# Performance work log

Hardware: AMD Instinct MI355X
Metric: run time of the kernel (lower is better)

Reference implementation:

```python
import jax, jax.numpy as jnp
import numpy as np

HEADS = 8
NEG_SLOPE = 0.2


def _layer_norm(x, g, b, eps=1e-5):
    mu = x.mean(-1, keepdims=True)
    var = ((x - mu) ** 2).mean(-1, keepdims=True)
    return (x - mu) / jnp.sqrt(var + eps) * g + b


def setup_inputs() -> dict:
    key = jax.random.key(0)
    ks = jax.random.split(key, 24)
    N, E, H, L = 512, 260000, 256, 4
    s = 0.05
    return dict(
        x=jax.random.normal(ks[0], (N, 1), jnp.float32),
        edge_index=jax.random.randint(ks[1], (2, E), 0, N),
        edge_attr=jax.random.uniform(ks[2], (E, 3), jnp.float32),
        emb_W=jax.random.normal(ks[3], (1, H)) * s,
        emb_b=jnp.zeros((H,)),
        Wl=jax.random.normal(ks[4], (L, H, H)) * s,
        bl=jnp.zeros((L, H)),
        Wr=jax.random.normal(ks[5], (L, H, H)) * s,
        br=jnp.zeros((L, H)),
        We=jax.random.normal(ks[6], (L, 3, H)) * s,
        att=jax.random.normal(ks[7], (L, HEADS, H // HEADS)) * s,
        gb=jnp.zeros((L, H)),
        ln_g=jnp.ones((L, H)),
        ln_b=jnp.zeros((L, H)),
        p1_W=jax.random.normal(ks[8], (2 * H, H)) * s,
        p1_b=jnp.zeros((H,)),
        p2_W=jax.random.normal(ks[9], (H, H // 2)) * s,
        p2_b=jnp.zeros((H // 2,)),
        p3_W=jax.random.normal(ks[10], (H // 2, 1)) * s,
        p3_b=jnp.zeros((1,)),
        v1_W=jax.random.normal(ks[11], (2 * H, H)) * s,
        v1_b=jnp.zeros((H,)),
        v2_W=jax.random.normal(ks[12], (H, 1)) * s,
        v2_b=jnp.zeros((1,)),
        coupling=jnp.asarray(1.0, jnp.float32),
    )


def reference(x, edge_index, edge_attr, emb_W, emb_b, Wl, bl, Wr, br, We, att,
              gb, ln_g, ln_b, p1_W, p1_b, p2_W, p2_b, p3_W, p3_b,
              v1_W, v1_b, v2_W, v2_b, coupling):
    N = x.shape[0]
    E = edge_attr.shape[0]
    L = Wl.shape[0]
    C = Wl.shape[-1] // HEADS
    src, dst = edge_index[0], edge_index[1]

    # PyG GATv2Conv adds self-loops with edge_attr fill_value='mean'
    # (mean of incoming edge_attr per destination node).
    sums = jax.ops.segment_sum(edge_attr, dst, num_segments=N)
    cnt = jax.ops.segment_sum(jnp.ones((E,), edge_attr.dtype), dst, num_segments=N)
    self_attr = sums / jnp.maximum(cnt, 1.0)[:, None]
    loop = jnp.arange(N)
    src_f = jnp.concatenate([src, loop])            # [E+N]
    dst_f = jnp.concatenate([dst, loop])
    ea_f = jnp.concatenate([edge_attr, self_attr])  # [E+N, 3]

    h = x @ emb_W + emb_b                           # [N, H]
    for l in range(L):
        res = h
        xl = (h @ Wl[l] + bl[l]).reshape(N, HEADS, C)
        xr = (h @ Wr[l] + br[l]).reshape(N, HEADS, C)
        ee = (ea_f @ We[l]).reshape(-1, HEADS, C)
        # GATv2 scoring: leaky_relu(x_l[src]+x_r[dst]+edge) . att
        m = jax.nn.leaky_relu(xl[src_f] + xr[dst_f] + ee, NEG_SLOPE)
        alpha = jnp.einsum('ehc,hc->eh', m, att[l])
        amax = jax.ops.segment_max(alpha, dst_f, num_segments=N)
        alpha = jnp.exp(alpha - amax[dst_f])
        denom = jax.ops.segment_sum(alpha, dst_f, num_segments=N)
        alpha = alpha / denom[dst_f]
        out = jax.ops.segment_sum(xl[src_f] * alpha[..., None], dst_f,
                                  num_segments=N).reshape(N, HEADS * C) + gb[l]
        h = jax.nn.relu(_layer_norm(out + res, ln_g[l], ln_b[l]))

    # graph-level representation (single graph, batch=None branch)
    graph_repr = jnp.concatenate([h.mean(0, keepdims=True),
                                  h.max(0, keepdims=True)], axis=1)  # [1, 2H]

    # all-pairs edge representations (i < j)
    iu, ju = jnp.triu_indices(N, k=1)
    er = jnp.concatenate([h[iu], h[ju]], axis=1)    # [N(N-1)/2, 2H]
    p = jax.nn.relu(er @ p1_W + p1_b)
    p = jax.nn.relu(p @ p2_W + p2_b)
    policy_logits = (p @ p3_W + p3_b).squeeze(-1)   # [N(N-1)/2]

    v = jax.nn.relu(graph_repr @ v1_W + v1_b)
    value = (v @ v2_W + v2_b).squeeze(-1)           # [1]

    # Potts energy: per-color degree-squared approximation of triangles
    colors = jnp.argmax(edge_attr, axis=1)
    energy = jnp.asarray(0.0, h.dtype)
    for c in (1, 2):
        w = (colors == c).astype(h.dtype)
        deg = (jax.ops.segment_sum(w, src, num_segments=N)
               + jax.ops.segment_sum(w, dst, num_segments=N))
        energy = energy + (deg ** 2).sum() / (2.0 * N)
    energy = energy * coupling

    return policy_logits, value, energy
```

## Files before the change

### kernel.cpp

```cpp
#include <hip/hip_runtime.h>
#include <math.h>

#define HDIM 256
#define NHEADS 8
#define NEG 0.2f
#define NB 64
#define SEG 4

typedef float f32x4 __attribute__((ext_vector_type(4)));
typedef _Float16 f16x8 __attribute__((ext_vector_type(8)));
typedef __fp16 fp16v2 __attribute__((ext_vector_type(2)));

__global__ __launch_bounds__(256) void edge_part(
    const int* __restrict__ ei, const float* __restrict__ ea, int E, int CH,
    int* __restrict__ pcnt, float* __restrict__ psum, int* __restrict__ pcol) {
  __shared__ int   lcnt[512];
  __shared__ float ls0[512], ls1[512], ls2[512];
  __shared__ int   lcol[1024];
  int t = threadIdx.x, b = blockIdx.x;
  for (int n = t; n < 512; n += 256) {
    lcnt[n] = 0; ls0[n] = 0.f; ls1[n] = 0.f; ls2[n] = 0.f;
    lcol[n] = 0; lcol[512 + n] = 0;
  }
  __syncthreads();
  int e0 = b * CH, e1 = min(E, e0 + CH);
  for (int e = e0 + t; e < e1; e += 256) {
    int src = ei[e], dst = ei[E + e];
    float a0 = ea[3*e], a1 = ea[3*e+1], a2 = ea[3*e+2];
    atomicAdd(&lcnt[dst], 1);
    atomicAdd(&ls0[dst], a0);
    atomicAdd(&ls1[dst], a1);
    atomicAdd(&ls2[dst], a2);
    int idx = 0; float best = a0;
    if (a1 > best) { best = a1; idx = 1; }
    if (a2 > best) { idx = 2; }
    if (idx) {
      int o = (idx - 1) << 9;
      atomicAdd(&lcol[o + src], 1);
      atomicAdd(&lcol[o + dst], 1);
    }
  }
  __syncthreads();
  for (int n = t; n < 512; n += 256) {
    pcnt[b*512 + n] = lcnt[n];
    psum[(size_t)(0*NB + b)*512 + n] = ls0[n];
    psum[(size_t)(1*NB + b)*512 + n] = ls1[n];
    psum[(size_t)(2*NB + b)*512 + n] = ls2[n];
    pcol[(size_t)(0*NB + b)*512 + n] = lcol[n];
    pcol[(size_t)(1*NB + b)*512 + n] = lcol[512 + n];
  }
}

__global__ __launch_bounds__(256) void red_kernel(
    const int* __restrict__ pcnt, const float* __restrict__ psum,
    const int* __restrict__ pcol,
    int* __restrict__ cnt, float* __restrict__ sred, int* __restrict__ dred,
    int* __restrict__ pbase) {
  int q = blockIdx.x >> 1;
  int n = (blockIdx.x & 1)*256 + threadIdx.x;
  if (q == 0) {
    int run = 0;
#pragma unroll 8
    for (int b = 0; b < NB; ++b) {
      int v = pcnt[b*512 + n];
      pbase[b*512 + n] = run;
      run += v;
    }
    cnt[n] = run;
  } else if (q <= 3) {
    int qq = q - 1;
    float s = 0.f;
#pragma unroll 8
    for (int b = 0; b < NB; ++b) s += psum[(size_t)(qq*NB + b)*512 + n];
    sred[qq*512 + n] = s;
  } else {
    int qq = q - 4;
    int s = 0;
#pragma unroll 8
    for (int b = 0; b < NB; ++b) s += pcol[(size_t)(qq*NB + b)*512 + n];
    dred[qq*512 + n] = s;
  }
}

__global__ __launch_bounds__(512) void scan2(
    const int* __restrict__ cnt, const float* __restrict__ sred,
    const int* __restrict__ dred, int N,
    int* __restrict__ rowp, float4* __restrict__ csr,
    const float* __restrict__ coupling, float* __restrict__ eout) {
  int t = threadIdx.x;
  int c = (t < N) ? cnt[t] : 0;
  __shared__ int sbuf[512];
  int v = (t < N) ? (c + 1) : 0;
  sbuf[t] = v;
  __syncthreads();
  for (int off = 1; off < 512; off <<= 1) {
    int add = (t >= off) ? sbuf[t - off] : 0;
    __syncthreads();
    sbuf[t] += add;
    __syncthreads();
  }
  int incl = sbuf[t], excl = incl - v;
  if (t < N) {
    rowp[t] = excl;
    if (t == N - 1) rowp[N] = incl;
    float inv = 1.f / fmaxf((float)c, 1.f);
    csr[excl] = make_float4(sred[t]*inv, sred[512 + t]*inv, sred[1024 + t]*inv,
                            __int_as_float(t));
  }
  float e = 0.f;
  if (t < N) {
    float d1 = (float)dred[t], d2 = (float)dred[512 + t];
    e = d1*d1 + d2*d2;
  }
#pragma unroll
  for (int off = 1; off < 64; off <<= 1) e += __shfl_xor(e, off);
  __shared__ float wred[8];
  if ((t & 63) == 0) wred[t >> 6] = e;
  __syncthreads();
  if (t == 0) {
    float s = 0.f;
#pragma unroll
    for (int i = 0; i < 8; ++i) s += wred[i];
    eout[0] = coupling[0] * s / (2.f * (float)N);
  }
}

__global__ __launch_bounds__(256) void scatter2(
    const int* __restrict__ ei, const float* __restrict__ ea, int E, int CH,
    const int* __restrict__ rowp, const int* __restrict__ pbase,
    float4* __restrict__ csr) {
  __shared__ int lofs[512];
  int t = threadIdx.x, b = blockIdx.x;
  for (int n = t; n < 512; n += 256) lofs[n] = 0;
  __syncthreads();
  int e0 = b * CH, e1 = min(E, e0 + CH);
  for (int e = e0 + t; e < e1; e += 256) {
    int src = ei[e], dst = ei[E + e];
    float a0 = ea[3*e], a1 = ea[3*e+1], a2 = ea[3*e+2];
    int lp = atomicAdd(&lofs[dst], 1);
    int pos = rowp[dst] + 1 + pbase[b*512 + dst] + lp;
    csr[pos] = make_float4(a0, a1, a2, __int_as_float(src));
  }
}

__global__ __launch_bounds__(256) void emb_kernel(
    const float* __restrict__ x, const float* __restrict__ eW,
    const float* __restrict__ eb, float* __restrict__ h) {
  int n = blockIdx.x, t = threadIdx.x;
  h[n*HDIM + t] = fmaf(x[n], eW[t], eb[t]);
}

__global__ __launch_bounds__(256) void dual_gemm(
    const float* __restrict__ Hm,
    const float* __restrict__ W1, const float* __restrict__ b1,
    const float* __restrict__ W2, const float* __restrict__ b2,
    float* __restrict__ o1, float* __restrict__ o2) {
  int t = threadIdx.x;
  int n0 = blockIdx.x * 2;
  __shared__ float sh[2][HDIM];
#pragma unroll
  for (int r = 0; r < 2; ++r) sh[r][t] = Hm[(size_t)(n0 + r)*HDIM + t];
  __syncthreads();
  float a[2] = {0.f,0.f}, b[2] = {0.f,0.f};
#pragma unroll 8
  for (int k = 0; k < HDIM; ++k) {
    float w1 = W1[(size_t)k*HDIM + t];
    float w2 = W2[(size_t)k*HDIM + t];
#pragma unroll
    for (int r = 0; r < 2; ++r) {
      a[r] = fmaf(sh[r][k], w1, a[r]);
      b[r] = fmaf(sh[r][k], w2, b[r]);
    }
  }
  float bb1 = b1 ? b1[t] : 0.f;
  float bb2 = b2 ? b2[t] : 0.f;
#pragma unroll
  for (int r = 0; r < 2; ++r) {
    o1[(size_t)(n0 + r)*HDIM + t] = a[r] + bb1;
    o2[(size_t)(n0 + r)*HDIM + t] = b[r] + bb2;
  }
}

__global__ __launch_bounds__(256) void attn_gather(
    const float* __restrict__ xl, const float* __restrict__ xr,
    const float4* __restrict__ csr, const int* __restrict__ row_start,
    const float* __restrict__ We, const float* __restrict__ att,
    float* __restrict__ pm, float* __restrict__ pl, float* __restrict__ pacc) {
  int nb = blockIdx.x;
  int n = nb >> 2, sgm = nb & (SEG - 1);
  int t = threadIdx.x;
  int g = t >> 5, l = t & 31, hd = l >> 2, qd = l & 3;
  int cb = hd*32 + qd*8;

  float xrv[8], w0[8], w1[8], w2[8], av[8];
#pragma unroll
  for (int j = 0; j < 8; ++j) {
    xrv[j] = xr[(size_t)n*HDIM + cb + j];
    w0[j]  = We[cb + j];
    w1[j]  = We[HDIM + cb + j];
    w2[j]  = We[2*HDIM + cb + j];
    av[j]  = att[cb + j];
  }
  int rs = row_start[n], re = row_start[n+1], len = re - rs;
  int s0 = rs + ((len * sgm) >> 2);
  int s1 = rs + ((len * (sgm + 1)) >> 2);

  float mh = -INFINITY, lh = 0.f;
  float acc[8] = {0.f,0.f,0.f,0.f,0.f,0.f,0.f,0.f};

  int idx = s0 + g;
  if (idx < s1) {
    float4 rec = csr[idx];
    while (idx < s1) {
      int idxn = idx + 8;
      float4 recn = csr[idxn < s1 ? idxn : rs];
      int s = __float_as_int(rec.w);
      const float* xp = xl + (size_t)s*HDIM + cb;
      float xv[8];
      float4 x0 = *(const float4*)xp;
      float4 x1 = *(const float4*)(xp + 4);
      xv[0]=x0.x; xv[1]=x0.y; xv[2]=x0.z; xv[3]=x0.w;
      xv[4]=x1.x; xv[5]=x1.y; xv[6]=x1.z; xv[7]=x1.w;
      float partial = 0.f;
#pragma unroll
      for (int j = 0; j < 8; ++j) {
        float m = fmaf(rec.z, w2[j], fmaf(rec.y, w1[j], fmaf(rec.x, w0[j], xrv[j]))) + xv[j];
        m = fmaxf(m, NEG * m);
        partial = fmaf(m, av[j], partial);
      }
      partial += __shfl_xor(partial, 1);
      partial += __shfl_xor(partial, 2);
      if (partial > mh) {
        float sc = __expf(mh - partial);
        lh *= sc;
#pragma unroll
        for (int j = 0; j < 8; ++j) acc[j] *= sc;
        mh = partial;
      }
      float pw = __expf(partial - mh);
      lh += pw;
#pragma unroll
      for (int j = 0; j < 8; ++j) acc[j] = fmaf(pw, xv[j], acc[j]);
      rec = recn; idx = idxn;
    }
  }

  __shared__ float lacc[8][HDIM];
  __shared__ float lm[8][NHEADS];
  __shared__ float llv[8][NHEADS];
#pragma unroll
  for (int j = 0; j < 8; ++j) lacc[g][cb + j] = acc[j];
  if (qd == 0) { lm[g][hd] = mh; llv[g][hd] = lh; }
  __syncthreads();

  int c = t, hh = c >> 5;
  float M = -INFINITY;
#pragma unroll
  for (int g2 = 0; g2 < 8; ++g2) M = fmaxf(M, lm[g2][hh]);
  float L = 0.f, o = 0.f;
#pragma unroll
  for (int g2 = 0; g2 < 8; ++g2) {
    float e2 = __expf(lm[g2][hh] - M);
    L = fmaf(llv[g2][hh], e2, L);
    o = fmaf(lacc[g2][c], e2, o);
  }
  pacc[(size_t)nb*HDIM + c] = o;
  if ((c & 31) == 0) {
    pm[nb*NHEADS + hh] = M;
    pl[nb*NHEADS + hh] = L;
  }
}

__global__ __launch_bounds__(256) void attn_merge(
    const float* __restrict__ pm, const float* __restrict__ pl,
    const float* __restrict__ pacc,
    const float* __restrict__ gb, const float* __restrict__ lng,
    const float* __restrict__ lnb,
    const float* __restrict__ h_in, float* __restrict__ h_out) {
  int n = blockIdx.x, t = threadIdx.x;
  int c = t, hh = c >> 5;
  float M = -INFINITY;
#pragma unroll
  for (int s = 0; s < SEG; ++s) M = fmaxf(M, pm[(n*SEG + s)*NHEADS + hh]);
  float L = 0.f, o = 0.f;
#pragma unroll
  for (int s = 0; s < SEG; ++s) {
    float e2 = __expf(pm[(n*SEG + s)*NHEADS + hh] - M);
    L = fmaf(pl[(n*SEG + s)*NHEADS + hh], e2, L);
    o = fmaf(pacc[(size_t)(n*SEG + s)*HDIM + c], e2, o);
  }
  float val = o / L + gb[c] + h_in[(size_t)n*HDIM + c];

  float s1 = val, s2 = val * val;
#pragma unroll
  for (int off = 1; off < 64; off <<= 1) {
    s1 += __shfl_xor(s1, off);
    s2 += __shfl_xor(s2, off);
  }
  __shared__ float rs1[4], rs2[4];
  if ((t & 63) == 0) { rs1[t >> 6] = s1; rs2[t >> 6] = s2; }
  __syncthreads();
  float S1 = rs1[0] + rs1[1] + rs1[2] + rs1[3];
  float S2 = rs2[0] + rs2[1] + rs2[2] + rs2[3];
  float mu = S1 * (1.f/HDIM);
  float var = S2 * (1.f/HDIM) - mu * mu;
  float y = (val - mu) * rsqrtf(var + 1e-5f);
  y = fmaf(y, lng[c], lnb[c]);
  h_out[(size_t)n*HDIM + c] = fmaxf(y, 0.f);
}

__global__ __launch_bounds__(256) void w2_prep_kernel(
    const float* __restrict__ W2, unsigned short* __restrict__ W2h) {
  int tid = blockIdx.x * 256 + threadIdx.x;
  int k = tid >> 7, n = tid & 127;
  int c = k >> 5, kq = (k >> 3) & 3, kj = k & 7;
  int nt = n >> 4, nl = n & 15;
  int lane = kq*16 + nl;
  _Float16 hv = (_Float16)W2[(size_t)k*128 + n];
  W2h[(size_t)(((c*8 + nt)*64 + lane)*8 + kj)] = *(unsigned short*)&hv;
}

__global__ __launch_bounds__(256, 4) void pair_mfma_kernel(
    const float* __restrict__ A, const float* __restrict__ Bm,
    const unsigned short* __restrict__ W2h,
    const float* __restrict__ b2, const float* __restrict__ W3,
    const float* __restrict__ b3, float* __restrict__ out, int N) {
  int bb = blockIdx.x;
  int half = bb & 1;
  int b = bb >> 1, ti = 0, rem = 32;
  while (b >= rem) { b -= rem; ti++; rem--; }
  int tj = ti + b;
  int i0 = ti * 16 + half * 8;
  int j0 = tj * 16;

  int t = threadIdx.x;
  int w = t >> 6, l = t & 63;
  int quad = l >> 4, nl = l & 15;

  float b2v[8], w3v[8];
#pragma unroll
  for (int nt = 0; nt < 8; ++nt) {
    b2v[nt] = b2[nt*16 + nl];
    w3v[nt] = W3[nt*16 + nl];
  }

  const float* Brow = Bm + (size_t)(j0 + nl) * HDIM;
  const float* Arow0 = A + (size_t)(i0 + w*2) * HDIM;

  f32x4 acc[2][8];
#pragma unroll
  for (int a2 = 0; a2 < 2; ++a2)
#pragma unroll
    for (int nt = 0; nt < 8; ++nt) acc[a2][nt] = (f32x4){0.f,0.f,0.f,0.f};

  for (int c = 0; c < 8; ++c) {
    int kb = c*32 + quad*8;
    float4 bv0 = *(const float4*)(Brow + kb);
    float4 bv1 = *(const float4*)(Brow + kb + 4);

    f16x8 afrag[2];
#pragma unroll
    for (int a2 = 0; a2 < 2; ++a2) {
      const float* Ar = Arow0 + (size_t)a2*HDIM + kb;
      float4 av0 = *(const float4*)Ar;
      float4 av1 = *(const float4*)(Ar + 4);
      union { f16x8 v8; fp16v2 v2[4]; } u;
      u.v2[0] = __builtin_amdgcn_cvt_pkrtz(fmaxf(av0.x + bv0.x, 0.f),
                                           fmaxf(av0.y + bv0.y, 0.f));
      u.v2[1] = __builtin_amdgcn_cvt_pkrtz(fmaxf(av0.z + bv0.z, 0.f),
                                           fmaxf(av0.w + bv0.w, 0.f));
      u.v2[2] = __builtin_amdgcn_cvt_pkrtz(fmaxf(av1.x + bv1.x, 0.f),
                                           fmaxf(av1.y + bv1.y, 0.f));
      u.v2[3] = __builtin_amdgcn_cvt_pkrtz(fmaxf(av1.z + bv1.z, 0.f),
                                           fmaxf(av1.w + bv1.w, 0.f));
      afrag[a2] = u.v8;
    }

#pragma unroll
    for (int nt = 0; nt < 8; ++nt) {
      f16x8 bfrag = *(const f16x8*)(W2h + (size_t)(((c*8 + nt)*64 + l) * 8));
#pragma unroll
      for (int a2 = 0; a2 < 2; ++a2)
        acc[a2][nt] = __builtin_amdgcn_mfma_f32_16x16x32_f16(
            afrag[a2], bfrag, acc[a2][nt], 0, 0, 0);
    }
  }

  float b3v = b3[0];
#pragma unroll
  for (int a2 = 0; a2 < 2; ++a2) {
    int i = i0 + w*2 + a2;
#pragma unroll
    for (int r = 0; r < 4; ++r) {
      float s = 0.f;
#pragma unroll
      for (int nt = 0; nt < 8; ++nt)
        s = fmaf(fmaxf(acc[a2][nt][r] + b2v[nt], 0.f), w3v[nt], s);
      s += __shfl_xor(s, 1);
      s += __shfl_xor(s, 2);
      s += __shfl_xor(s, 4);
      s += __shfl_xor(s, 8);
      if (nl == 0) {
        int j = j0 + quad*4 + r;
        if (i < j)
          out[(size_t)i*(2*N - i - 1)/2 + (j - i - 1)] = s + b3v;
      }
    }
  }
}

__global__ __launch_bounds__(256) void pool_kernel(
    const float* __restrict__ h, float* __restrict__ psums,
    float* __restrict__ pmaxs) {
  int g = blockIdx.x, t = threadIdx.x;
  float s = 0.f, m = -INFINITY;
#pragma unroll
  for (int r = 0; r < 16; ++r) {
    float v = h[(size_t)(g*16 + r)*HDIM + t];
    s += v; m = fmaxf(m, v);
  }
  psums[g*HDIM + t] = s;
  pmaxs[g*HDIM + t] = m;
}

__global__ __launch_bounds__(256) void value1_kernel(
    const float* __restrict__ psums, const float* __restrict__ pmaxs,
    const float* __restrict__ v1W, float* __restrict__ vpart, int N) {
  int b = blockIdx.x, t = threadIdx.x;
  int k0 = b * 16;
  int kk = t >> 4, g = t & 15;
  __shared__ float repr16[16];
  int k = k0 + kk;
  float v;
  if (k < HDIM) {
    v = psums[g*HDIM + k] + psums[(g + 16)*HDIM + k];
    v += __shfl_xor(v, 1); v += __shfl_xor(v, 2);
    v += __shfl_xor(v, 4); v += __shfl_xor(v, 8);
    if (g == 0) repr16[kk] = v / (float)N;
  } else {
    int kc = k - HDIM;
    v = fmaxf(pmaxs[g*HDIM + kc], pmaxs[(g + 16)*HDIM + kc]);
    v = fmaxf(v, __shfl_xor(v, 1)); v = fmaxf(v, __shfl_xor(v, 2));
    v = fmaxf(v, __shfl_xor(v, 4)); v = fmaxf(v, __shfl_xor(v, 8));
    if (g == 0) repr16[kk] = v;
  }
  __syncthreads();
  float pv = 0.f;
#pragma unroll
  for (int q = 0; q < 16; ++q)
    pv = fmaf(repr16[q], v1W[(size_t)(k0 + q)*HDIM + t], pv);
  vpart[b*HDIM + t] = pv;
}

__global__ __launch_bounds__(256) void value2_kernel(
    const float* __restrict__ vpart, const float* __restrict__ v1b,
    const float* __restrict__ v2W, const float* __restrict__ v2b,
    float* __restrict__ out) {
  int t = threadIdx.x;
  float a = 0.f;
#pragma unroll
  for (int g = 0; g < 32; ++g) a += vpart[g*HDIM + t];
  a = fmaxf(a + v1b[t], 0.f);
  float pv = a * v2W[t];
#pragma unroll
  for (int off = 1; off < 64; off <<= 1) pv += __shfl_xor(pv, off);
  __shared__ float wsum[4];
  if ((t & 63) == 0) wsum[t >> 6] = pv;
  __syncthreads();
  if (t == 0) out[0] = wsum[0] + wsum[1] + wsum[2] + wsum[3] + v2b[0];
}

extern "C" void kernel_launch(void* const* d_in, const int* in_sizes, int n_in,
                              void* d_out, int out_size, void* d_ws, size_t ws_size,
                              hipStream_t stream) {
  const float* x    = (const float*)d_in[0];
  const int*   ei   = (const int*)  d_in[1];
  const float* ea   = (const float*)d_in[2];
  const float* embW = (const float*)d_in[3];
  const float* embb = (const float*)d_in[4];
  const float* Wl   = (const float*)d_in[5];
  const float* bl   = (const float*)d_in[6];
  const float* Wr   = (const float*)d_in[7];
  const float* br   = (const float*)d_in[8];
  const float* We   = (const float*)d_in[9];
  const float* att  = (const float*)d_in[10];
  const float* gb   = (const float*)d_in[11];
  const float* lng  = (const float*)d_in[12];
  const float* lnb  = (const float*)d_in[13];
  const float* p1W  = (const float*)d_in[14];
  const float* p1b  = (const float*)d_in[15];
  const float* p2W  = (const float*)d_in[16];
  const float* p2b  = (const float*)d_in[17];
  const float* p3W  = (const float*)d_in[18];
  const float* p3b  = (const float*)d_in[19];
  const float* v1W  = (const float*)d_in[20];
  const float* v1b  = (const float*)d_in[21];
  const float* v2W  = (const float*)d_in[22];
  const float* v2b  = (const float*)d_in[23];
  const float* coup = (const float*)d_in[24];

  int N = in_sizes[0];
  int E = in_sizes[2] / 3;
  float* out = (float*)d_out;
  size_t P = (size_t)N*(N-1)/2;

  char* w = (char*)d_ws;
  int*    rowp = (int*)   (w + 0);
  float*  plS  = (float*) (w + 2560);
  float*  plM  = (float*) (w + 35328);
  float*  vprt = (float*) (w + 68096);
  float4* csr  = (float4*)(w + 101120);
  size_t csr_end = 101120 + (size_t)(E + N) * 16;
  csr_end = (csr_end + 255) & ~(size_t)255;
  float* hA  = (float*)(w + csr_end);
  float* hB  = hA  + (size_t)N*HDIM;
  float* xlb = hB  + (size_t)N*HDIM;
  float* xrb = xlb + (size_t)N*HDIM;
  float* Ab  = xrb + (size_t)N*HDIM;
  float* Bb  = Ab  + (size_t)N*HDIM;
  unsigned short* W2h = (unsigned short*)(Bb + (size_t)N*HDIM);
  size_t ubase = ((size_t)((char*)(W2h + 32768) - w) + 255) & ~(size_t)255;

  char* U = w + ubase;
  int*    pcnt = (int*)   (U + 0);
  float*  psum = (float*) (U + 131072);
  int*    pcol = (int*)   (U + 524288);
  int*    pbase= (int*)   (U + 786432);
  int*    cnt  = (int*)   (U + 917504);
  float*  sred = (float*) (U + 919552);
  int*    dred = (int*)   (U + 925696);
  float*  pmv  = (float*) (U + 0);
  float*  plv  = (float*) (U + 65536);
  float*  pacc = (float*) (U + 131072);

  int CH = (E + NB - 1) / NB;
  edge_part<<<NB, 256, 0, stream>>>(ei, ea, E, CH, pcnt, psum, pcol);
  red_kernel<<<12, 256, 0, stream>>>(pcnt, psum, pcol, cnt, sred, dred, pbase);
  scan2<<<1, 512, 0, stream>>>(cnt, sred, dred, N, rowp, csr, coup, out + P + 1);
  scatter2<<<NB, 256, 0, stream>>>(ei, ea, E, CH, rowp, pbase, csr);
  emb_kernel<<<N, 256, 0, stream>>>(x, embW, embb, hA);
  w2_prep_kernel<<<128, 256, 0, stream>>>(p2W, W2h);

  float* hin = hA;
  float* hout = hB;
  for (int l = 0; l < 4; ++l) {
    dual_gemm<<<N/2, 256, 0, stream>>>(hin,
        Wl + (size_t)l*HDIM*HDIM, bl + l*HDIM,
        Wr + (size_t)l*HDIM*HDIM, br + l*HDIM, xlb, xrb);
    attn_gather<<<N*SEG, 256, 0, stream>>>(xlb, xrb, csr, rowp,
        We + (size_t)l*3*HDIM, att + (size_t)l*HDIM, pmv, plv, pacc);
    attn_merge<<<N, 256, 0, stream>>>(pmv, plv, pacc,
        gb + (size_t)l*HDIM, lng + (size_t)l*HDIM, lnb + (size_t)l*HDIM,
        hin, hout);
    float* tmp = hin; hin = hout; hout = tmp;
  }

  dual_gemm<<<N/2, 256, 0, stream>>>(hin, p1W, p1b,
      p1W + (size_t)HDIM*HDIM, (const float*)nullptr, Ab, Bb);

  pair_mfma_kernel<<<1056, 256, 0, stream>>>(Ab, Bb, W2h, p2b, p3W, p3b, out, N);

  pool_kernel<<<32, 256, 0, stream>>>(hin, plS, plM);
  value1_kernel<<<32, 256, 0, stream>>>(plS, plM, v1W, vprt, N);
  value2_kernel<<<1, 256, 0, stream>>>(vprt, v1b, v2W, v2b, out + P);
}
```

Baseline: 351.3 us.

## Use fp16 MFMA for per-layer dual GEMMs with pre-swizzled weights

Replaces the scalar fp32 dual_gemm with an MFMA 16x16x32 fp16 kernel. A new prep kernel converts all Wl, Wr and p1 weights once into fp16 in the MFMA B-fragment layout. Activations are converted to fp16 on the fly with round-toward-zero packing. This targets the five small 512x256x256 GEMM pairs, at the cost of an extra prep launch and reduced precision in the node projections.

Result: faster. 319.5 us (-9.0%).

```diff
diff --git a/kernel.cpp b/kernel.cpp
--- a/kernel.cpp
+++ b/kernel.cpp
@@ -150,35 +150,57 @@
   h[n*HDIM + t] = fmaf(x[n], eW[t], eb[t]);
 }
 
-__global__ __launch_bounds__(256) void dual_gemm(
+__global__ __launch_bounds__(256) void w_prep_all(
+    const float* __restrict__ Wl, const float* __restrict__ Wr,
+    const float* __restrict__ p1W, unsigned short* __restrict__ dst) {
+  int gid = blockIdx.x * 256 + threadIdx.x;
+  int s = gid >> 16, e = gid & 65535;
+  int k = e >> 8, n = e & 255;
+  const float* src = (s < 4) ? (Wl + (size_t)s*65536)
+                   : (s < 8) ? (Wr + (size_t)(s-4)*65536)
+                             : (p1W + (size_t)(s-8)*65536);
+  int c = k >> 5, quad = (k >> 3) & 3, kj = k & 7;
+  int nt = n >> 4, nl = n & 15;
+  int lane = quad*16 + nl;
+  _Float16 hv = (_Float16)src[(size_t)k*256 + n];
+  dst[(size_t)s*65536 + ((nt*8 + c)*512 + lane*8 + kj)] = *(unsigned short*)&hv;
+}
+
+__global__ __launch_bounds__(256) void dual_gemm_mfma(
     const float* __restrict__ Hm,
-    const float* __restrict__ W1, const float* __restrict__ b1,
-    const float* __restrict__ W2, const float* __restrict__ b2,
+    const unsigned short* __restrict__ W1h, const unsigned short* __restrict__ W2h,
+    const float* __restrict__ b1, const float* __restrict__ b2,
     float* __restrict__ o1, float* __restrict__ o2) {
-  int t = threadIdx.x;
-  int n0 = blockIdx.x * 2;
-  __shared__ float sh[2][HDIM];
-#pragma unroll
-  for (int r = 0; r < 2; ++r) sh[r][t] = Hm[(size_t)(n0 + r)*HDIM + t];
-  __syncthreads();
-  float a[2] = {0.f,0.f}, b[2] = {0.f,0.f};
-#pragma unroll 8
-  for (int k = 0; k < HDIM; ++k) {
-    float w1 = W1[(size_t)k*HDIM + t];
-    float w2 = W2[(size_t)k*HDIM + t];
-#pragma unroll
-    for (int r = 0; r < 2; ++r) {
-      a[r] = fmaf(sh[r][k], w1, a[r]);
-      b[r] = fmaf(sh[r][k], w2, b[r]);
-    }
-  }
-  float bb1 = b1 ? b1[t] : 0.f;
-  float bb2 = b2 ? b2[t] : 0.f;
-#pragma unroll
-  for (int r = 0; r < 2; ++r) {
-    o1[(size_t)(n0 + r)*HDIM + t] = a[r] + bb1;
-    o2[(size_t)(n0 + r)*HDIM + t] = b[r] + bb2;
-  }
+  int bx = blockIdx.x, by = blockIdx.y;
+  int t = threadIdx.x, w = t >> 6, l = t & 63;
+  int quad = l >> 4, nl = l & 15;
+  int mt = bx*4 + w;
+
+  const unsigned short* Wh; const float* bias; float* o; int nt;
+  if (by < 16) { Wh = W1h; bias = b1; o = o1; nt = by; }
+  else         { Wh = W2h; bias = b2; o = o2; nt = by - 16; }
+
+  const float* Ar = Hm + (size_t)(mt*16 + nl)*HDIM + quad*8;
+  f32x4 acc = (f32x4){0.f, 0.f, 0.f, 0.f};
+
+#pragma unroll
+  for (int c = 0; c < 8; ++c) {
+    float4 a0 = *(const float4*)(Ar + c*32);
+    float4 a1 = *(const float4*)(Ar + c*32 + 4);
+    union { f16x8 v8; fp16v2 v2[4]; } u;
+    u.v2[0] = __builtin_amdgcn_cvt_pkrtz(a0.x, a0.y);
+    u.v2[1] = __builtin_amdgcn_cvt_pkrtz(a0.z, a0.w);
+    u.v2[2] = __builtin_amdgcn_cvt_pkrtz(a1.x, a1.y);
+    u.v2[3] = __builtin_amdgcn_cvt_pkrtz(a1.z, a1.w);
+    f16x8 bfrag = *(const f16x8*)(Wh + (size_t)((nt*8 + c)*512 + l*8));
+    acc = __builtin_amdgcn_mfma_f32_16x16x32_f16(u.v8, bfrag, acc, 0, 0, 0);
+  }
+
+  int colg = nt*16 + nl;
+  float bv = bias ? bias[colg] : 0.f;
+#pragma unroll
+  for (int r = 0; r < 4; ++r)
+    o[(size_t)(mt*16 + quad*4 + r)*HDIM + colg] = acc[r] + bv;
 }
 
 __global__ __launch_bounds__(256) void attn_gather(
@@ -518,8 +540,9 @@
   float* xrb = xlb + (size_t)N*HDIM;
   float* Ab  = xrb + (size_t)N*HDIM;
   float* Bb  = Ab  + (size_t)N*HDIM;
-  unsigned short* W2h = (unsigned short*)(Bb + (size_t)N*HDIM);
-  size_t ubase = ((size_t)((char*)(W2h + 32768) - w) + 255) & ~(size_t)255;
+  unsigned short* W2h   = (unsigned short*)(Bb + (size_t)N*HDIM);
+  unsigned short* Whall = W2h + 32768;
+  size_t ubase = ((size_t)((char*)(Whall + 10*65536) - w) + 255) & ~(size_t)255;
 
   char* U = w + ubase;
   int*    pcnt = (int*)   (U + 0);
@@ -540,13 +563,14 @@
   scatter2<<<NB, 256, 0, stream>>>(ei, ea, E, CH, rowp, pbase, csr);
   emb_kernel<<<N, 256, 0, stream>>>(x, embW, embb, hA);
   w2_prep_kernel<<<128, 256, 0, stream>>>(p2W, W2h);
+  w_prep_all<<<2560, 256, 0, stream>>>(Wl, Wr, p1W, Whall);
 
   float* hin = hA;
   float* hout = hB;
   for (int l = 0; l < 4; ++l) {
-    dual_gemm<<<N/2, 256, 0, stream>>>(hin,
-        Wl + (size_t)l*HDIM*HDIM, bl + l*HDIM,
-        Wr + (size_t)l*HDIM*HDIM, br + l*HDIM, xlb, xrb);
+    dual_gemm_mfma<<<dim3(8, 32), 256, 0, stream>>>(hin,
+        Whall + (size_t)l*65536, Whall + (size_t)(4 + l)*65536,
+        bl + l*HDIM, br + l*HDIM, xlb, xrb);
     attn_gather<<<N*SEG, 256, 0, stream>>>(xlb, xrb, csr, rowp,
         We + (size_t)l*3*HDIM, att + (size_t)l*HDIM, pmv, plv, pacc);
     attn_merge<<<N, 256, 0, stream>>>(pmv, plv, pacc,
@@ -555,8 +579,9 @@
     float* tmp = hin; hin = hout; hout = tmp;
   }
 
-  dual_gemm<<<N/2, 256, 0, stream>>>(hin, p1W, p1b,
-      p1W + (size_t)HDIM*HDIM, (const float*)nullptr, Ab, Bb);
+  dual_gemm_mfma<<<dim3(8, 32), 256, 0, stream>>>(hin,
+      Whall + (size_t)8*65536, Whall + (size_t)9*65536,
+      p1b, (const float*)nullptr, Ab, Bb);
 
   pair_mfma_kernel<<<1056, 256, 0, stream>>>(Ab, Bb, W2h, p2b, p3W, p3b, out, N);
 
```
